# Performance work log

Measured on AMD Instinct MI355X. Metric: run time of the kernel, lower is better.

## Reference

```python
import jax, jax.numpy as jnp
import numpy as np

G = 10            # int(2 / 0.2) BEV grid side
NUM_PILLARS = G * G
INTERVAL = 0.2
BN_EPS = 1e-5


def setup_inputs() -> dict:
    key = jax.random.key(0)
    ks = jax.random.split(key, 8)
    B, N = 8, 20000
    x = jax.random.normal(ks[0], (B, N, 3), dtype=jnp.float32)
    # Linear weights stored as [in, out] (torch Linear applies x @ W.T); no biases.
    W1 = jax.random.normal(ks[1], (6, 32), dtype=jnp.float32) * 0.1
    W2 = jax.random.normal(ks[2], (32, 64), dtype=jnp.float32) * 0.1
    W3 = jax.random.normal(ks[3], (64, 128), dtype=jnp.float32) * 0.1
    W4 = jax.random.normal(ks[4], (256, 768), dtype=jnp.float32) * 0.05
    bn_gamma = jnp.ones((NUM_PILLARS,), dtype=jnp.float32)
    bn_beta = jnp.zeros((NUM_PILLARS,), dtype=jnp.float32)
    return {"x": x, "W1": W1, "W2": W2, "W3": W3, "W4": W4,
            "bn_gamma": bn_gamma, "bn_beta": bn_beta}


def _encode_sample(p, seg, W1, W2, W3, W4):
    # p: [N,3] swapped coords (Z,Y,X); seg: [N] pillar id in [0,100)
    N = p.shape[0]
    counts = jax.ops.segment_sum(jnp.ones((N,), p.dtype), seg, num_segments=NUM_PILLARS)  # [100]
    cent = jax.ops.segment_sum(p, seg, num_segments=NUM_PILLARS) / jnp.maximum(counts, 1.0)[:, None]
    aug = jnp.concatenate([p, p - cent[seg]], axis=-1)          # [N,6]
    h = jax.nn.relu(aug @ W1)
    h = jax.nn.relu(h @ W2)
    h = jax.nn.relu(h @ W3)                                      # [N,128]
    pil = jax.ops.segment_max(h, seg, num_segments=NUM_PILLARS)  # [100,128] (-inf on empty, never gathered)
    h2 = jnp.concatenate([h, pil[seg]], axis=-1)                 # [N,256]
    h2 = jax.nn.relu(h2 @ W4)                                    # [N,768]
    enc = jax.ops.segment_max(h2, seg, num_segments=NUM_PILLARS) # [100,768]
    return jnp.where(counts[:, None] > 0, enc, 0.0)             # empty pillars stay zero


def reference(x, W1, W2, W3, W4, bn_gamma, bn_beta):
    # column swap [Y,Z,X] -> [Z,Y,X]
    pts = jnp.stack([x[..., 1], x[..., 0], x[..., 2]], axis=-1)  # [B,N,3]
    # pillar indices from (Y, X) = swapped cols 1:3
    yx = jnp.clip(pts[..., 1:] + 1.0, 0.0, 1.99)
    idx = jnp.floor(yx / INTERVAL).astype(jnp.int32)             # trunc == floor (non-negative)
    seg = idx[..., 0] * G + idx[..., 1]                          # [B,N], matches flatten(2) order y*10+x
    feat = jax.vmap(lambda p, s: _encode_sample(p, s, W1, W2, W3, W4))(pts, seg)  # [B,100,768]
    # BatchNorm1d(100) in training mode over [B, 100, 768]: stats over dims (0,2)
    mean = feat.mean(axis=(0, 2))
    var = feat.var(axis=(0, 2))  # biased variance, as torch uses for normalization
    out = (feat - mean[None, :, None]) * jax.lax.rsqrt(var + BN_EPS)[None, :, None]
    return out * bn_gamma[None, :, None] + bn_beta[None, :, None]
```

## Files before the change

kernel.cpp:

```cpp
#include <hip/hip_runtime.h>
#include <stdint.h>

#define B_    8
#define N_    20000
#define NPTS  (B_*N_)
#define G_    10
#define NPIL  100
#define NSB   (B_*NPIL)
#define BN_EPS 1e-5f

#define OFF_COUNTS   0
#define OFF_SUMS     3200
#define OFF_STARTS   12800
#define ZERO_BYTES   16320
#define OFF_CENT     19264
#define OFF_SEG      28864
#define OFF_W3BF     668864
#define OFF_W4T      709824
#define OFF_PILW4B   1307840
#define OFF_H3P      3765440
#define WS_NEED      44725440

typedef __attribute__((ext_vector_type(8))) short bf16x8;
typedef __attribute__((ext_vector_type(4))) float f32x4;

typedef const __attribute__((address_space(1))) void gas_void;
typedef __attribute__((address_space(3))) void las_void;

__device__ __forceinline__ void gload_lds16(const void* g, void* l){
    __builtin_amdgcn_global_load_lds((gas_void*)g, (las_void*)l, 16, 0, 0);
}

__device__ __forceinline__ int binidx(float v){
    float t = v + 1.0f;
    t = fminf(fmaxf(t, 0.0f), 1.99f);
    return (int)(t / 0.2f);
}
__device__ __forceinline__ unsigned short f2bf(float f){
    unsigned u = __float_as_uint(f);
    u += 0x7fffu + ((u >> 16) & 1u);
    return (unsigned short)(u >> 16);
}
__device__ __forceinline__ unsigned u16max2(unsigned a, unsigned b){
    unsigned ah=a>>16, bh=b>>16, al=a&0xffffu, bl=b&0xffffu;
    return ((ah>bh?ah:bh)<<16) | (al>bl?al:bl);
}
__device__ __forceinline__ uint4 max16(uint4 a, uint4 b){
    uint4 r; r.x=u16max2(a.x,b.x); r.y=u16max2(a.y,b.y);
    r.z=u16max2(a.z,b.z); r.w=u16max2(a.w,b.w); return r;
}

__global__ __launch_bounds__(256) void kA(const float* __restrict__ x,
                                          int* __restrict__ segrank,
                                          int* __restrict__ counts,
                                          float* __restrict__ sums){
    __shared__ int   lc[NPIL];
    __shared__ float lsum[NPIL*3];
    __shared__ int   lbase[NPIL];
    int tid = threadIdx.x;
    if (tid < NPIL){
        lc[tid] = 0;
        lsum[3*tid] = 0.f; lsum[3*tid+1] = 0.f; lsum[3*tid+2] = 0.f;
    }
    __syncthreads();
    int i0  = blockIdx.x * 625;
    int bat = i0 / N_;
    int sv[3], lrv[3];
    #pragma unroll
    for (int t = 0; t < 3; t++){
        int ii = tid + t*256;
        int i  = i0 + ii;
        sv[t] = -1;
        if (ii < 625){
            float x0 = x[3*i], x1 = x[3*i+1], x2 = x[3*i+2];
            int s = binidx(x0)*G_ + binidx(x2);
            sv[t] = s;
            lrv[t] = atomicAdd(&lc[s], 1);
            atomicAdd(&lsum[s*3+0], x1);
            atomicAdd(&lsum[s*3+1], x0);
            atomicAdd(&lsum[s*3+2], x2);
        }
    }
    __syncthreads();
    if (tid < NPIL){
        int c = lc[tid];
        if (c > 0){
            int sb = bat*NPIL + tid;
            lbase[tid] = atomicAdd(&counts[sb], c);
            atomicAdd(&sums[3*sb+0], lsum[3*tid+0]);
            atomicAdd(&sums[3*sb+1], lsum[3*tid+1]);
            atomicAdd(&sums[3*sb+2], lsum[3*tid+2]);
        }
    }
    __syncthreads();
    #pragma unroll
    for (int t = 0; t < 3; t++){
        if (sv[t] >= 0){
            int i = i0 + tid + t*256;
            segrank[i] = (bat*NPIL + sv[t]) | ((lbase[sv[t]] + lrv[t]) << 10);
        }
    }
}

__global__ __launch_bounds__(1024) void kScan(const int* __restrict__ counts,
                                              int* __restrict__ starts){
    __shared__ int s[1024];
    int t = threadIdx.x;
    int c = (t < NSB) ? counts[t] : 0;
    s[t] = c;
    __syncthreads();
    for (int off=1; off<1024; off<<=1){
        int v = (t >= off) ? s[t-off] : 0;
        __syncthreads();
        s[t] += v;
        __syncthreads();
    }
    if (t < NSB) starts[t] = s[t]-c;
    if (t == NSB) starts[NSB] = s[NSB-1];
}

__global__ __launch_bounds__(256) void kB(const int* __restrict__ counts,
                                          const float* __restrict__ sums,
                                          float* __restrict__ cent,
                                          const float* __restrict__ W3,
                                          unsigned short* __restrict__ W3bf,
                                          const float* __restrict__ W4,
                                          unsigned short* __restrict__ W4T){
    int idx = blockIdx.x*256 + threadIdx.x;
    if (idx < 2400){
        cent[idx] = sums[idx] / fmaxf((float)counts[idx/3], 1.0f);
    } else if (idx < 2400 + 8192){
        int t = idx - 2400;
        int col = t >> 6, k = t & 63;
        W3bf[t] = f2bf(W3[k*128 + col]);
    } else if (idx < 2400 + 8192 + 196608){
        int t = idx - 2400 - 8192;
        int k = t / 768, j = t - k*768;
        W4T[j*256 + k] = f2bf(W4[t]);
    }
}

__global__ __launch_bounds__(256) void kC12(const float* __restrict__ x,
                                            const int* __restrict__ segrank,
                                            const int* __restrict__ starts,
                                            const float* __restrict__ cent,
                                            const float* __restrict__ W1,
                                            const float* __restrict__ W2,
                                            unsigned short* __restrict__ h3p){
    int i = blockIdx.x*256 + threadIdx.x;
    if (i >= NPTS) return;
    int pk = segrank[i];
    int sb = pk & 1023;
    int pos = starts[sb] + (pk >> 10);
    float p0 = x[3*i+1], p1 = x[3*i], p2 = x[3*i+2];
    float aug[6];
    aug[0]=p0; aug[1]=p1; aug[2]=p2;
    aug[3]=p0-cent[sb*3+0]; aug[4]=p1-cent[sb*3+1]; aug[5]=p2-cent[sb*3+2];

    float h1[32];
    #pragma unroll
    for (int j=0;j<32;j++){
        float a = 0.f;
        #pragma unroll
        for (int k=0;k<6;k++) a += aug[k]*W1[k*32+j];
        h1[j] = fmaxf(a, 0.f);
    }
    unsigned buf[32];
    #pragma unroll 8
    for (int jp=0;jp<32;jp++){
        float a0 = 0.f, a1 = 0.f;
        #pragma unroll
        for (int k=0;k<32;k++){
            a0 += h1[k]*W2[k*64 + jp*2];
            a1 += h1[k]*W2[k*64 + jp*2 + 1];
        }
        buf[jp] = (unsigned)f2bf(fmaxf(a0,0.f)) | ((unsigned)f2bf(fmaxf(a1,0.f)) << 16);
    }
    uint4* d4 = (uint4*)(h3p + (size_t)pos*128 + 64);
    #pragma unroll
    for (int q=0;q<8;q++) d4[q] = ((const uint4*)buf)[q];
}

__global__ __launch_bounds__(512) void kC3(const unsigned short* __restrict__ W3bf,
                                           unsigned short* __restrict__ h3p){
    __shared__ unsigned short Al[256*64];
    __shared__ unsigned short Bl[128*64];
    int tid = threadIdx.x;
    int m0  = blockIdx.x * 256;
    #pragma unroll
    for (int it=0; it<4; it++){
        int cc = tid + it*512;
        int row = cc >> 3, ch = cc & 7;
        int chs = ch ^ (row & 7);
        gload_lds16(h3p + (size_t)(m0+row)*128 + 64 + chs*8, (char*)Al + cc*16);
    }
    #pragma unroll
    for (int it=0; it<2; it++){
        int cc = tid + it*512;
        int row = cc >> 3, ch = cc & 7;
        int chs = ch ^ (row & 7);
        gload_lds16(W3bf + (size_t)row*64 + chs*8, (char*)Bl + cc*16);
    }
    __syncthreads();

    int lane = tid & 63, wid = tid >> 6;
    int wm = wid >> 1, wn = wid & 1;
    int l15 = lane & 15, lhi = lane >> 4;

    f32x4 acc[4][4];
    #pragma unroll
    for (int m=0;m<4;m++)
        #pragma unroll
        for (int n=0;n<4;n++) acc[m][n] = (f32x4){0.f,0.f,0.f,0.f};

    #pragma unroll
    for (int kk=0; kk<2; kk++){
        bf16x8 af[4], bfr[4];
        #pragma unroll
        for (int f=0; f<4; f++){
            int ra = wm*64 + f*16 + l15;
            af[f]  = *(const bf16x8*)((char*)Al + ra*128 + (((kk*4+lhi) ^ (ra&7))*16));
            int rb = wn*64 + f*16 + l15;
            bfr[f] = *(const bf16x8*)((char*)Bl + rb*128 + (((kk*4+lhi) ^ (rb&7))*16));
        }
        #pragma unroll
        for (int m=0;m<4;m++)
            #pragma unroll
            for (int n=0;n<4;n++)
                acc[m][n] = __builtin_amdgcn_mfma_f32_16x16x32_bf16(af[m], bfr[n], acc[m][n], 0,0,0);
    }

    #pragma unroll
    for (int m=0;m<4;m++)
        #pragma unroll
        for (int r=0;r<4;r++){
            int row = m0 + wm*64 + m*16 + lhi*4 + r;
            #pragma unroll
            for (int n=0;n<4;n++){
                int col = wn*64 + n*16 + l15;
                h3p[(size_t)row*128 + col] = f2bf(fmaxf(acc[m][n][r], 0.f));
            }
        }
}

__global__ __launch_bounds__(256) void kMB(const unsigned short* __restrict__ h3p,
                                           const int* __restrict__ starts,
                                           const unsigned short* __restrict__ W4T,
                                           float* __restrict__ pilW4b){
    __shared__ uint4 sd[16][16];
    __shared__ unsigned short pill[128];
    int sb = blockIdx.x;
    int tid = threadIdx.x;
    int tx = tid & 15, ty = tid >> 4;
    int s = starts[sb], npts = starts[sb+1] - s;
    uint4 acc = {0u,0u,0u,0u};
    for (int p = ty; p < npts; p += 16){
        uint4 v = *(const uint4*)(h3p + (size_t)(s+p)*128 + tx*8);
        acc = max16(acc, v);
    }
    sd[ty][tx] = acc;
    __syncthreads();
    #pragma unroll
    for (int off=8; off; off>>=1){
        if (ty < off) sd[ty][tx] = max16(sd[ty][tx], sd[ty+off][tx]);
        __syncthreads();
    }
    if (ty == 0) *(uint4*)(pill + tx*8) = sd[0][tx];
    __syncthreads();
    #pragma unroll
    for (int c=0;c<3;c++){
        int col = tid + c*256;
        const unsigned short* w = W4T + (size_t)col*256 + 128;
        float bsum = 0.f;
        #pragma unroll
        for (int q=0;q<16;q++){
            uint4 wv = *(const uint4*)(w + q*8);
            const unsigned short* wl = (const unsigned short*)&wv;
            #pragma unroll
            for (int e=0;e<8;e++)
                bsum += __uint_as_float(((unsigned)wl[e])<<16)
                      * __uint_as_float(((unsigned)pill[q*8+e])<<16);
        }
        pilW4b[(size_t)sb*768 + col] = bsum;
    }
}

__global__ __launch_bounds__(256, 3) void kD(const unsigned short* __restrict__ h3p,
                                             const int* __restrict__ starts,
                                             const float* __restrict__ pilW4b,
                                             const unsigned short* __restrict__ W4T,
                                             float* __restrict__ out){
    __shared__ unsigned short Al[64*128];
    __shared__ float red[2][2][64];
    int nt = blockIdx.x >> 7;
    int g  = blockIdx.x & 127;
    int n0 = nt * 128;
    int tid = threadIdx.x;
    int lane = tid & 63, wid = tid >> 6;
    int wm = wid >> 1, wn = wid & 1;
    int l15 = lane & 15, lhi = lane >> 4;

    bf16x8 bfr[4][4];
    #pragma unroll
    for (int kk=0;kk<4;kk++)
        #pragma unroll
        for (int n=0;n<4;n++){
            int rb = n0 + wn*64 + n*16 + l15;
            bfr[kk][n] = *(const bf16x8*)(W4T + (size_t)rb*256 + (kk*4+lhi)*8);
        }

    int arow[4], achs[4];
    #pragma unroll
    for (int it=0;it<4;it++){
        int cc = tid + it*256;
        arow[it] = cc >> 4;
        achs[it] = (cc & 15) ^ (arow[it] & 15);
    }

    for (int sb = g; sb < NSB; sb += 128){
        int start = starts[sb];
        int npts  = starts[sb+1] - start;
        if (npts == 0){
            if (tid < 128) out[(size_t)sb*768 + n0 + tid] = 0.f;
            continue;
        }
        const unsigned short* asrc[4];
        #pragma unroll
        for (int it=0;it<4;it++)
            asrc[it] = h3p + (size_t)(start+arow[it])*128 + achs[it]*8;

        float mx[2][4][4];
        #pragma unroll
        for (int m=0;m<2;m++)
            #pragma unroll
            for (int n=0;n<4;n++)
                #pragma unroll
                for (int r=0;r<4;r++) mx[m][n][r] = -3.0e38f;

        int nfull = npts >> 6;
        int tailr = npts & 63;

        for (int c=0; c<nfull; c++){
            __syncthreads();
            #pragma unroll
            for (int it=0; it<4; it++){
                gload_lds16(asrc[it], (char*)Al + (tid + it*256)*16);
                asrc[it] += 64*128;
            }
            __syncthreads();
            f32x4 acc[2][4];
            #pragma unroll
            for (int m=0;m<2;m++)
                #pragma unroll
                for (int n=0;n<4;n++) acc[m][n] = (f32x4){0.f,0.f,0.f,0.f};
            #pragma unroll
            for (int kk=0; kk<4; kk++){
                bf16x8 af[2];
                #pragma unroll
                for (int f=0; f<2; f++){
                    int ra = wm*32 + f*16 + l15;
                    af[f] = *(const bf16x8*)((const char*)Al + ra*256 + (((kk*4+lhi) ^ (ra&15))*16));
                }
                #pragma unroll
                for (int m=0;m<2;m++)
                    #pragma unroll
                    for (int n=0;n<4;n++)
                        acc[m][n] = __builtin_amdgcn_mfma_f32_16x16x32_bf16(af[m], bfr[kk][n], acc[m][n], 0,0,0);
            }
            #pragma unroll
            for (int m=0;m<2;m++)
                #pragma unroll
                for (int n=0;n<4;n++)
                    #pragma unroll
                    for (int r=0;r<4;r++)
                        mx[m][n][r] = fmaxf(mx[m][n][r], acc[m][n][r]);
        }
        if (tailr > 0){
            int base = nfull << 6;
            __syncthreads();
            #pragma unroll
            for (int it=0; it<4; it++){
                int idx = start + base + arow[it];
                idx = idx < NPTS ? idx : NPTS-1;
                gload_lds16(h3p + (size_t)idx*128 + achs[it]*8, (char*)Al + (tid + it*256)*16);
            }
            __syncthreads();
            f32x4 acc[2][4];
            #pragma unroll
            for (int m=0;m<2;m++)
                #pragma unroll
                for (int n=0;n<4;n++) acc[m][n] = (f32x4){0.f,0.f,0.f,0.f};
            #pragma unroll
            for (int kk=0; kk<4; kk++){
                bf16x8 af[2];
                #pragma unroll
                for (int f=0; f<2; f++){
                    int ra = wm*32 + f*16 + l15;
                    af[f] = *(const bf16x8*)((const char*)Al + ra*256 + (((kk*4+lhi) ^ (ra&15))*16));
                }
                #pragma unroll
                for (int m=0;m<2;m++)
                    #pragma unroll
                    for (int n=0;n<4;n++)
                        acc[m][n] = __builtin_amdgcn_mfma_f32_16x16x32_bf16(af[m], bfr[kk][n], acc[m][n], 0,0,0);
            }
            #pragma unroll
            for (int m=0;m<2;m++)
                #pragma unroll
                for (int r=0;r<4;r++){
                    int p = wm*32 + m*16 + lhi*4 + r;
                    if (p < tailr){
                        #pragma unroll
                        for (int n=0;n<4;n++)
                            mx[m][n][r] = fmaxf(mx[m][n][r], acc[m][n][r]);
                    }
                }
        }

        float red4[4];
        #pragma unroll
        for (int n=0;n<4;n++){
            float v = -3.0e38f;
            #pragma unroll
            for (int m=0;m<2;m++)
                #pragma unroll
                for (int r=0;r<4;r++) v = fmaxf(v, mx[m][n][r]);
            v = fmaxf(v, __shfl_xor(v, 16));
            v = fmaxf(v, __shfl_xor(v, 32));
            red4[n] = v;
        }
        if (lhi == 0){
            #pragma unroll
            for (int n=0;n<4;n++) red[wm][wn][n*16 + l15] = red4[n];
        }
        __syncthreads();
        if (wm == 0){
            float v = fmaxf(red[0][wn][lane], red[1][wn][lane]);
            int col = n0 + wn*64 + lane;
            v = fmaxf(v + pilW4b[(size_t)sb*768 + col], 0.f);
            out[(size_t)sb*768 + col] = v;
        }
    }
}

__global__ __launch_bounds__(256) void kE(float* __restrict__ out,
                                          const float* __restrict__ gamma,
                                          const float* __restrict__ beta){
    int p = blockIdx.x;
    int tid = threadIdx.x;
    float v[B_*3];
    float sum = 0.f, ssq = 0.f;
    #pragma unroll
    for (int b=0;b<B_;b++)
        #pragma unroll
        for (int r=0;r<3;r++){
            float t = out[(b*NPIL + p)*768 + tid + r*256];
            v[b*3+r] = t;
            sum += t; ssq += t*t;
        }
    #pragma unroll
    for (int off=32; off; off>>=1){
        sum += __shfl_xor(sum, off);
        ssq += __shfl_xor(ssq, off);
    }
    __shared__ float ls[8];
    __shared__ float sc[2];
    int lane = tid & 63, w = tid >> 6;
    if (lane == 0){ ls[w] = sum; ls[4+w] = ssq; }
    __syncthreads();
    if (tid == 0){
        float S = ls[0]+ls[1]+ls[2]+ls[3];
        float Q = ls[4]+ls[5]+ls[6]+ls[7];
        float mean = S * (1.0f/6144.0f);
        float var  = Q * (1.0f/6144.0f) - mean*mean;
        float scale = rsqrtf(var + BN_EPS) * gamma[p];
        sc[0] = scale;
        sc[1] = beta[p] - mean*scale;
    }
    __syncthreads();
    float scale = sc[0], shift = sc[1];
    #pragma unroll
    for (int b=0;b<B_;b++)
        #pragma unroll
        for (int r=0;r<3;r++)
            out[(b*NPIL + p)*768 + tid + r*256] = v[b*3+r]*scale + shift;
}

extern "C" void kernel_launch(void* const* d_in, const int* in_sizes, int n_in,
                              void* d_out, int out_size, void* d_ws, size_t ws_size,
                              hipStream_t stream){
    if (ws_size < (size_t)WS_NEED) return;
    const float* x     = (const float*)d_in[0];
    const float* W1    = (const float*)d_in[1];
    const float* W2    = (const float*)d_in[2];
    const float* W3    = (const float*)d_in[3];
    const float* W4    = (const float*)d_in[4];
    const float* gamma = (const float*)d_in[5];
    const float* beta  = (const float*)d_in[6];
    float* out = (float*)d_out;
    char*  ws  = (char*)d_ws;

    int*            counts = (int*)           (ws + OFF_COUNTS);
    float*          sums   = (float*)         (ws + OFF_SUMS);
    int*            starts = (int*)           (ws + OFF_STARTS);
    float*          cent   = (float*)         (ws + OFF_CENT);
    int*            segrank= (int*)           (ws + OFF_SEG);
    unsigned short* W3bf   = (unsigned short*)(ws + OFF_W3BF);
    unsigned short* W4T    = (unsigned short*)(ws + OFF_W4T);
    float*          pilW4b = (float*)         (ws + OFF_PILW4B);
    unsigned short* h3p    = (unsigned short*)(ws + OFF_H3P);

    hipMemsetAsync(d_ws, 0, ZERO_BYTES, stream);

    kA<<<256, 256, 0, stream>>>(x, segrank, counts, sums);
    kScan<<<1, 1024, 0, stream>>>(counts, starts);
    kB<<<(2400+8192+196608+255)/256, 256, 0, stream>>>(counts, sums, cent, W3, W3bf, W4, W4T);
    kC12<<<(NPTS+255)/256, 256, 0, stream>>>(x, segrank, starts, cent, W1, W2, h3p);
    kC3<<<NPTS/256, 512, 0, stream>>>(W3bf, h3p);
    kMB<<<NSB, 256, 0, stream>>>(h3p, starts, W4T, pilW4b);
    kD<<<768, 256, 0, stream>>>(h3p, starts, pilW4b, W4T, out);
    kE<<<NPIL, 256, 0, stream>>>(out, gamma, beta);
}
```

Measured before the change: 201.5 us.

## Fold kB into kA/kScan and give kD one block per segment-tile with LDS weights

New measurement: 182.3 us. 1.11x faster.

```diff
diff --git a/kernel.cpp b/kernel.cpp
--- a/kernel.cpp
+++ b/kernel.cpp
@@ -53,17 +53,34 @@
 __global__ __launch_bounds__(256) void kA(const float* __restrict__ x,
                                           int* __restrict__ segrank,
                                           int* __restrict__ counts,
-                                          float* __restrict__ sums){
+                                          float* __restrict__ sums,
+                                          const float* __restrict__ W3,
+                                          unsigned short* __restrict__ W3bf,
+                                          const float* __restrict__ W4,
+                                          unsigned short* __restrict__ W4T){
+    int blk = blockIdx.x;
+    int tid = threadIdx.x;
+    if (blk >= 256){
+        int idx = (blk-256)*256 + tid;
+        if (idx < 8192){
+            int col = idx >> 6, k = idx & 63;
+            W3bf[idx] = f2bf(W3[k*128 + col]);
+        } else {
+            int t = idx - 8192;
+            int k = t / 768, j = t - k*768;
+            W4T[j*256 + k] = f2bf(W4[t]);
+        }
+        return;
+    }
     __shared__ int   lc[NPIL];
     __shared__ float lsum[NPIL*3];
     __shared__ int   lbase[NPIL];
-    int tid = threadIdx.x;
     if (tid < NPIL){
         lc[tid] = 0;
         lsum[3*tid] = 0.f; lsum[3*tid+1] = 0.f; lsum[3*tid+2] = 0.f;
     }
     __syncthreads();
-    int i0  = blockIdx.x * 625;
+    int i0  = blk * 625;
     int bat = i0 / N_;
     int sv[3], lrv[3];
     #pragma unroll
@@ -103,7 +120,9 @@
 }
 
 __global__ __launch_bounds__(1024) void kScan(const int* __restrict__ counts,
-                                              int* __restrict__ starts){
+                                              const float* __restrict__ sums,
+                                              int* __restrict__ starts,
+                                              float* __restrict__ cent){
     __shared__ int s[1024];
     int t = threadIdx.x;
     int c = (t < NSB) ? counts[t] : 0;
@@ -117,27 +136,8 @@
     }
     if (t < NSB) starts[t] = s[t]-c;
     if (t == NSB) starts[NSB] = s[NSB-1];
-}
-
-__global__ __launch_bounds__(256) void kB(const int* __restrict__ counts,
-                                          const float* __restrict__ sums,
-                                          float* __restrict__ cent,
-                                          const float* __restrict__ W3,
-                                          unsigned short* __restrict__ W3bf,
-                                          const float* __restrict__ W4,
-                                          unsigned short* __restrict__ W4T){
-    int idx = blockIdx.x*256 + threadIdx.x;
-    if (idx < 2400){
+    for (int idx = t; idx < 2400; idx += 1024)
         cent[idx] = sums[idx] / fmaxf((float)counts[idx/3], 1.0f);
-    } else if (idx < 2400 + 8192){
-        int t = idx - 2400;
-        int col = t >> 6, k = t & 63;
-        W3bf[t] = f2bf(W3[k*128 + col]);
-    } else if (idx < 2400 + 8192 + 196608){
-        int t = idx - 2400 - 8192;
-        int k = t / 768, j = t - k*768;
-        W4T[j*256 + k] = f2bf(W4[t]);
-    }
 }
 
 __global__ __launch_bounds__(256) void kC12(const float* __restrict__ x,
@@ -285,161 +285,167 @@
     }
 }
 
-__global__ __launch_bounds__(256, 3) void kD(const unsigned short* __restrict__ h3p,
-                                             const int* __restrict__ starts,
-                                             const float* __restrict__ pilW4b,
-                                             const unsigned short* __restrict__ W4T,
-                                             float* __restrict__ out){
+__global__ __launch_bounds__(256) void kD(const unsigned short* __restrict__ h3p,
+                                          const int* __restrict__ starts,
+                                          const float* __restrict__ pilW4b,
+                                          const unsigned short* __restrict__ W4T,
+                                          float* __restrict__ out){
     __shared__ unsigned short Al[64*128];
+    __shared__ unsigned short Bl[128*128];
     __shared__ float red[2][2][64];
-    int nt = blockIdx.x >> 7;
-    int g  = blockIdx.x & 127;
+    int b  = blockIdx.x;
+    int x_ = b & 7, t_ = b >> 3;
+    int k_ = t_ / 6, nt = t_ - k_*6;
+    int sb = x_ + 8*k_;
     int n0 = nt * 128;
     int tid = threadIdx.x;
+    int start = starts[sb];
+    int npts  = starts[sb+1] - start;
+    if (npts == 0){
+        if (tid < 128) out[(size_t)sb*768 + n0 + tid] = 0.f;
+        return;
+    }
+    #pragma unroll
+    for (int it=0; it<8; it++){
+        int cc = tid + it*256;
+        int row = cc >> 4, ch = cc & 15;
+        int chs = ch ^ (row & 15);
+        gload_lds16(W4T + (size_t)(n0+row)*256 + chs*8, (char*)Bl + cc*16);
+    }
+    const unsigned short* asrc[4];
+    int arow[4], achs[4];
+    #pragma unroll
+    for (int it=0; it<4; it++){
+        int cc = tid + it*256;
+        int row = cc >> 4, ch = cc & 15;
+        arow[it] = row;
+        achs[it] = ch ^ (row & 15);
+        asrc[it] = h3p + (size_t)(start+row)*128 + achs[it]*8;
+    }
     int lane = tid & 63, wid = tid >> 6;
     int wm = wid >> 1, wn = wid & 1;
     int l15 = lane & 15, lhi = lane >> 4;
 
-    bf16x8 bfr[4][4];
-    #pragma unroll
-    for (int kk=0;kk<4;kk++)
-        #pragma unroll
-        for (int n=0;n<4;n++){
-            int rb = n0 + wn*64 + n*16 + l15;
-            bfr[kk][n] = *(const bf16x8*)(W4T + (size_t)rb*256 + (kk*4+lhi)*8);
-        }
-
-    int arow[4], achs[4];
-    #pragma unroll
-    for (int it=0;it<4;it++){
-        int cc = tid + it*256;
-        arow[it] = cc >> 4;
-        achs[it] = (cc & 15) ^ (arow[it] & 15);
-    }
-
-    for (int sb = g; sb < NSB; sb += 128){
-        int start = starts[sb];
-        int npts  = starts[sb+1] - start;
-        if (npts == 0){
-            if (tid < 128) out[(size_t)sb*768 + n0 + tid] = 0.f;
-            continue;
-        }
-        const unsigned short* asrc[4];
-        #pragma unroll
-        for (int it=0;it<4;it++)
-            asrc[it] = h3p + (size_t)(start+arow[it])*128 + achs[it]*8;
-
-        float mx[2][4][4];
+    float mx[2][4][4];
+    #pragma unroll
+    for (int m=0;m<2;m++)
+        #pragma unroll
+        for (int n=0;n<4;n++)
+            #pragma unroll
+            for (int r=0;r<4;r++) mx[m][n][r] = -3.0e38f;
+
+    int nfull = npts >> 6;
+    int tailr = npts & 63;
+
+    for (int c=0; c<nfull; c++){
+        __syncthreads();
+        #pragma unroll
+        for (int it=0; it<4; it++){
+            gload_lds16(asrc[it], (char*)Al + (tid + it*256)*16);
+            asrc[it] += 64*128;
+        }
+        __syncthreads();
+        f32x4 acc[2][4];
         #pragma unroll
         for (int m=0;m<2;m++)
             #pragma unroll
-            for (int n=0;n<4;n++)
-                #pragma unroll
-                for (int r=0;r<4;r++) mx[m][n][r] = -3.0e38f;
-
-        int nfull = npts >> 6;
-        int tailr = npts & 63;
-
-        for (int c=0; c<nfull; c++){
-            __syncthreads();
-            #pragma unroll
-            for (int it=0; it<4; it++){
-                gload_lds16(asrc[it], (char*)Al + (tid + it*256)*16);
-                asrc[it] += 64*128;
+            for (int n=0;n<4;n++) acc[m][n] = (f32x4){0.f,0.f,0.f,0.f};
+        #pragma unroll
+        for (int kk=0; kk<4; kk++){
+            bf16x8 af[2], bfr[4];
+            #pragma unroll
+            for (int f=0; f<2; f++){
+                int ra = wm*32 + f*16 + l15;
+                af[f] = *(const bf16x8*)((const char*)Al + ra*256 + (((kk*4+lhi) ^ (ra&15))*16));
             }
-            __syncthreads();
-            f32x4 acc[2][4];
-            #pragma unroll
-            for (int m=0;m<2;m++)
-                #pragma unroll
-                for (int n=0;n<4;n++) acc[m][n] = (f32x4){0.f,0.f,0.f,0.f};
-            #pragma unroll
-            for (int kk=0; kk<4; kk++){
-                bf16x8 af[2];
-                #pragma unroll
-                for (int f=0; f<2; f++){
-                    int ra = wm*32 + f*16 + l15;
-                    af[f] = *(const bf16x8*)((const char*)Al + ra*256 + (((kk*4+lhi) ^ (ra&15))*16));
-                }
-                #pragma unroll
-                for (int m=0;m<2;m++)
-                    #pragma unroll
-                    for (int n=0;n<4;n++)
-                        acc[m][n] = __builtin_amdgcn_mfma_f32_16x16x32_bf16(af[m], bfr[kk][n], acc[m][n], 0,0,0);
+            #pragma unroll
+            for (int f=0; f<4; f++){
+                int rb = wn*64 + f*16 + l15;
+                bfr[f] = *(const bf16x8*)((const char*)Bl + rb*256 + (((kk*4+lhi) ^ (rb&15))*16));
             }
             #pragma unroll
             for (int m=0;m<2;m++)
                 #pragma unroll
                 for (int n=0;n<4;n++)
-                    #pragma unroll
-                    for (int r=0;r<4;r++)
-                        mx[m][n][r] = fmaxf(mx[m][n][r], acc[m][n][r]);
-        }
-        if (tailr > 0){
-            int base = nfull << 6;
-            __syncthreads();
-            #pragma unroll
-            for (int it=0; it<4; it++){
-                int idx = start + base + arow[it];
-                idx = idx < NPTS ? idx : NPTS-1;
-                gload_lds16(h3p + (size_t)idx*128 + achs[it]*8, (char*)Al + (tid + it*256)*16);
+                    acc[m][n] = __builtin_amdgcn_mfma_f32_16x16x32_bf16(af[m], bfr[n], acc[m][n], 0,0,0);
+        }
+        #pragma unroll
+        for (int m=0;m<2;m++)
+            #pragma unroll
+            for (int n=0;n<4;n++)
+                #pragma unroll
+                for (int r=0;r<4;r++)
+                    mx[m][n][r] = fmaxf(mx[m][n][r], acc[m][n][r]);
+    }
+    if (tailr > 0){
+        int base = nfull << 6;
+        __syncthreads();
+        #pragma unroll
+        for (int it=0; it<4; it++){
+            int idx = start + base + arow[it];
+            idx = idx < NPTS ? idx : NPTS-1;
+            gload_lds16(h3p + (size_t)idx*128 + achs[it]*8, (char*)Al + (tid + it*256)*16);
+        }
+        __syncthreads();
+        f32x4 acc[2][4];
+        #pragma unroll
+        for (int m=0;m<2;m++)
+            #pragma unroll
+            for (int n=0;n<4;n++) acc[m][n] = (f32x4){0.f,0.f,0.f,0.f};
+        #pragma unroll
+        for (int kk=0; kk<4; kk++){
+            bf16x8 af[2], bfr[4];
+            #pragma unroll
+            for (int f=0; f<2; f++){
+                int ra = wm*32 + f*16 + l15;
+                af[f] = *(const bf16x8*)((const char*)Al + ra*256 + (((kk*4+lhi) ^ (ra&15))*16));
             }
-            __syncthreads();
-            f32x4 acc[2][4];
+            #pragma unroll
+            for (int f=0; f<4; f++){
+                int rb = wn*64 + f*16 + l15;
+                bfr[f] = *(const bf16x8*)((const char*)Bl + rb*256 + (((kk*4+lhi) ^ (rb&15))*16));
+            }
             #pragma unroll
             for (int m=0;m<2;m++)
                 #pragma unroll
-                for (int n=0;n<4;n++) acc[m][n] = (f32x4){0.f,0.f,0.f,0.f};
-            #pragma unroll
-            for (int kk=0; kk<4; kk++){
-                bf16x8 af[2];
-                #pragma unroll
-                for (int f=0; f<2; f++){
-                    int ra = wm*32 + f*16 + l15;
-                    af[f] = *(const bf16x8*)((const char*)Al + ra*256 + (((kk*4+lhi) ^ (ra&15))*16));
-                }
-                #pragma unroll
-                for (int m=0;m<2;m++)
+                for (int n=0;n<4;n++)
+                    acc[m][n] = __builtin_amdgcn_mfma_f32_16x16x32_bf16(af[m], bfr[n], acc[m][n], 0,0,0);
+        }
+        #pragma unroll
+        for (int m=0;m<2;m++)
+            #pragma unroll
+            for (int r=0;r<4;r++){
+                int p = wm*32 + m*16 + lhi*4 + r;
+                if (p < tailr){
                     #pragma unroll
                     for (int n=0;n<4;n++)
-                        acc[m][n] = __builtin_amdgcn_mfma_f32_16x16x32_bf16(af[m], bfr[kk][n], acc[m][n], 0,0,0);
+                        mx[m][n][r] = fmaxf(mx[m][n][r], acc[m][n][r]);
+                }
             }
-            #pragma unroll
-            for (int m=0;m<2;m++)
-                #pragma unroll
-                for (int r=0;r<4;r++){
-                    int p = wm*32 + m*16 + lhi*4 + r;
-                    if (p < tailr){
-                        #pragma unroll
-                        for (int n=0;n<4;n++)
-                            mx[m][n][r] = fmaxf(mx[m][n][r], acc[m][n][r]);
-                    }
-                }
-        }
-
-        float red4[4];
-        #pragma unroll
-        for (int n=0;n<4;n++){
-            float v = -3.0e38f;
-            #pragma unroll
-            for (int m=0;m<2;m++)
-                #pragma unroll
-                for (int r=0;r<4;r++) v = fmaxf(v, mx[m][n][r]);
-            v = fmaxf(v, __shfl_xor(v, 16));
-            v = fmaxf(v, __shfl_xor(v, 32));
-            red4[n] = v;
-        }
-        if (lhi == 0){
-            #pragma unroll
-            for (int n=0;n<4;n++) red[wm][wn][n*16 + l15] = red4[n];
-        }
-        __syncthreads();
-        if (wm == 0){
-            float v = fmaxf(red[0][wn][lane], red[1][wn][lane]);
-            int col = n0 + wn*64 + lane;
-            v = fmaxf(v + pilW4b[(size_t)sb*768 + col], 0.f);
-            out[(size_t)sb*768 + col] = v;
-        }
+    }
+
+    float red4[4];
+    #pragma unroll
+    for (int n=0;n<4;n++){
+        float v = -3.0e38f;
+        #pragma unroll
+        for (int m=0;m<2;m++)
+            #pragma unroll
+            for (int r=0;r<4;r++) v = fmaxf(v, mx[m][n][r]);
+        v = fmaxf(v, __shfl_xor(v, 16));
+        v = fmaxf(v, __shfl_xor(v, 32));
+        red4[n] = v;
+    }
+    if (lhi == 0){
+        #pragma unroll
+        for (int n=0;n<4;n++) red[wm][wn][n*16 + l15] = red4[n];
+    }
+    __syncthreads();
+    if (wm == 0){
+        float v = fmaxf(red[0][wn][lane], red[1][wn][lane]);
+        int col = n0 + wn*64 + lane;
+        v = fmaxf(v + pilW4b[(size_t)sb*768 + col], 0.f);
+        out[(size_t)sb*768 + col] = v;
     }
 }
 
@@ -512,12 +518,11 @@
 
     hipMemsetAsync(d_ws, 0, ZERO_BYTES, stream);
 
-    kA<<<256, 256, 0, stream>>>(x, segrank, counts, sums);
-    kScan<<<1, 1024, 0, stream>>>(counts, starts);
-    kB<<<(2400+8192+196608+255)/256, 256, 0, stream>>>(counts, sums, cent, W3, W3bf, W4, W4T);
+    kA<<<1056, 256, 0, stream>>>(x, segrank, counts, sums, W3, W3bf, W4, W4T);
+    kScan<<<1, 1024, 0, stream>>>(counts, sums, starts, cent);
     kC12<<<(NPTS+255)/256, 256, 0, stream>>>(x, segrank, starts, cent, W1, W2, h3p);
     kC3<<<NPTS/256, 512, 0, stream>>>(W3bf, h3p);
     kMB<<<NSB, 256, 0, stream>>>(h3p, starts, W4T, pilW4b);
-    kD<<<768, 256, 0, stream>>>(h3p, starts, pilW4b, W4T, out);
+    kD<<<4800, 256, 0, stream>>>(h3p, starts, pilW4b, W4T, out);
     kE<<<NPIL, 256, 0, stream>>>(out, gamma, beta);
 }
```
